# Kernel tuning notes

Measured on AMD Instinct MI355X. Metric: run time of the kernel, lower is better.

## Reference

```python
import jax, jax.numpy as jnp
import numpy as np

NEG_INF = -1e30

def _pool_unpool(x, k):
    # x: [B, C, H, W]. Non-overlapping max pool with window k (floor-mode,
    # matching torch MaxPool2d default), then MaxUnpool: scatter the pooled max
    # back to its argmax location within each window, zeros elsewhere.
    B, C, H, W = x.shape
    Hc, Wc = (H // k) * k, (W // k) * k  # cropped region covered by windows
    xc = x[:, :, :Hc, :Wc]
    # reshape into windows: [B, C, H/k, k, W/k, k] -> [B, C, H/k, W/k, k*k]
    xw = xc.reshape(B, C, Hc // k, k, Wc // k, k).transpose(0, 1, 2, 4, 3, 5)
    xw = xw.reshape(B, C, Hc // k, Wc // k, k * k)
    mx = jnp.max(xw, axis=-1, keepdims=True)
    am = jnp.argmax(xw, axis=-1)  # first max index, matches torch tie-breaking
    onehot = (jnp.arange(k * k) == am[..., None])
    yw = jnp.where(onehot, mx, jnp.zeros_like(mx))
    yc = yw.reshape(B, C, Hc // k, Wc // k, k, k).transpose(0, 1, 2, 4, 3, 5)
    yc = yc.reshape(B, C, Hc, Wc)
    # output_size=size in torch unpool -> pad uncovered border with zeros
    return jnp.pad(yc, ((0, 0), (0, 0), (0, H - Hc), (0, W - Wc)))

def setup_inputs() -> dict:
    key = jax.random.key(0)
    x = jax.random.uniform(key, (16, 1, 1080, 1920), dtype=jnp.float32)
    return {"x": x}

def reference(x):
    k = 3
    x = _pool_unpool(x, k)
    x = _pool_unpool(x, k + 2)
    x = _pool_unpool(x, k + 3)
    return x
```

## Files before the change

kernel.cpp:

```cpp
#include <hip/hip_runtime.h>


#define IMG_H 1080
#define IMG_W 1920
#define TILE_H 30
#define TILE_W 240
#define NTHREADS 256

template <int K>
__device__ __forceinline__ void nms_stage(float (*tile)[TILE_W], int t) {
    constexpr int NWR = TILE_H / K;
    constexpr int NWC = TILE_W / K;
    for (int w = t; w < NWR * NWC; w += NTHREADS) {
        const int wr = w / NWC;
        const int wc = w - wr * NWC;
        const int r0 = wr * K;
        const int c0 = wc * K;
        float mx = -1.0f;
        int am = 0;
#pragma unroll
        for (int r = 0; r < K; ++r)
#pragma unroll
            for (int c = 0; c < K; ++c) {
                const float v = tile[r0 + r][c0 + c];
                if (v > mx) { mx = v; am = r * K + c; }
            }
#pragma unroll
        for (int r = 0; r < K; ++r)
#pragma unroll
            for (int c = 0; c < K; ++c)
                tile[r0 + r][c0 + c] = (r * K + c == am) ? mx : 0.0f;
    }
    __syncthreads();
}

__global__ __launch_bounds__(NTHREADS) void pooling_nms_kernel(
    const float* __restrict__ x, float* __restrict__ out) {
    __shared__ float tile[TILE_H][TILE_W];

    const int t = threadIdx.x;
    const int col0 = blockIdx.x * TILE_W;
    const int row0 = blockIdx.y * TILE_H;
    const size_t base = (size_t)blockIdx.z * (IMG_H * (size_t)IMG_W) +
                        (size_t)row0 * IMG_W + col0;
    const float* src = x + base;
    float* dst = out + base;

    constexpr int VPR = TILE_W / 4;
    constexpr int NV = TILE_H * VPR;
    for (int i = t; i < NV; i += NTHREADS) {
        const int r = i / VPR;
        const int c4 = i - r * VPR;
        const float4 v =
            *reinterpret_cast<const float4*>(src + (size_t)r * IMG_W + c4 * 4);
        *reinterpret_cast<float4*>(&tile[r][c4 * 4]) = v;
    }
    __syncthreads();

    nms_stage<3>(tile, t);
    nms_stage<5>(tile, t);
    nms_stage<6>(tile, t);

    for (int i = t; i < NV; i += NTHREADS) {
        const int r = i / VPR;
        const int c4 = i - r * VPR;
        *reinterpret_cast<float4*>(dst + (size_t)r * IMG_W + c4 * 4) =
            *reinterpret_cast<const float4*>(&tile[r][c4 * 4]);
    }
}

extern "C" void kernel_launch(void* const* d_in, const int* in_sizes, int n_in,
                              void* d_out, int out_size, void* d_ws, size_t ws_size,
                              hipStream_t stream) {
    const float* x = (const float*)d_in[0];
    float* out = (float*)d_out;
    dim3 grid(IMG_W / TILE_W, IMG_H / TILE_H, 16);
    pooling_nms_kernel<<<grid, NTHREADS, 0, stream>>>(x, out);
}
```

Measured before the change: 238.8 us.

## Replace dense tile stages with sparse argmax-candidate cascade across pooling levels

Instead of staging the full tile in shared memory and rewriting it after each pool/unpool stage, the kernel computes 3x3 window maxima and positions directly from global memory. The 5x5 and 6x6 stages then operate only on sparse (value, position) candidates held in shared memory. The output tile is zero-filled and only the surviving maxima are scattered back. This removes the dense shared-memory read/write passes, at the cost of uncoalesced strided global reads and scattered single-element stores, plus added tie-breaking logic to stay exact.

```diff
diff --git a/kernel.cpp b/kernel.cpp
--- a/kernel.cpp
+++ b/kernel.cpp
@@ -5,67 +5,94 @@
 #define IMG_W 1920
 #define TILE_H 30
 #define TILE_W 240
-#define NTHREADS 256
+#define NT 256
 
-template <int K>
-__device__ __forceinline__ void nms_stage(float (*tile)[TILE_W], int t) {
-    constexpr int NWR = TILE_H / K;
-    constexpr int NWC = TILE_W / K;
-    for (int w = t; w < NWR * NWC; w += NTHREADS) {
-        const int wr = w / NWC;
-        const int wc = w - wr * NWC;
-        const int r0 = wr * K;
-        const int c0 = wc * K;
+__global__ __launch_bounds__(NT) void pooling_nms_kernel(
+    const float* __restrict__ x, float* __restrict__ out) {
+    __shared__ float sval[800];
+    __shared__ int   spos[800];
+    __shared__ float w5val[288];
+    __shared__ int   w5pos[288];
+
+    const int t = threadIdx.x;
+    const size_t base = (size_t)blockIdx.z * ((size_t)IMG_H * IMG_W) +
+                        (size_t)blockIdx.y * TILE_H * IMG_W +
+                        (size_t)blockIdx.x * TILE_W;
+    const float* src = x + base;
+    float* dst = out + base;
+
+    for (int w = t; w < 800; w += NT) {
+        const int wr = w / 80;
+        const int wc = w - wr * 80;
+        const int r0 = wr * 3, c0 = wc * 3;
         float mx = -1.0f;
         int am = 0;
 #pragma unroll
-        for (int r = 0; r < K; ++r)
-#pragma unroll
-            for (int c = 0; c < K; ++c) {
-                const float v = tile[r0 + r][c0 + c];
-                if (v > mx) { mx = v; am = r * K + c; }
-            }
-#pragma unroll
-        for (int r = 0; r < K; ++r)
-#pragma unroll
-            for (int c = 0; c < K; ++c)
-                tile[r0 + r][c0 + c] = (r * K + c == am) ? mx : 0.0f;
+        for (int r = 0; r < 3; ++r) {
+            const float* p = src + (size_t)(r0 + r) * IMG_W + c0;
+            const float v0 = p[0], v1 = p[1], v2 = p[2];
+            if (v0 > mx) { mx = v0; am = ((r0 + r) << 8) | c0; }
+            if (v1 > mx) { mx = v1; am = ((r0 + r) << 8) | (c0 + 1); }
+            if (v2 > mx) { mx = v2; am = ((r0 + r) << 8) | (c0 + 2); }
+        }
+        sval[w] = mx;
+        spos[w] = am;
     }
-    __syncthreads();
-}
 
-__global__ __launch_bounds__(NTHREADS) void pooling_nms_kernel(
-    const float* __restrict__ x, float* __restrict__ out) {
-    __shared__ float tile[TILE_H][TILE_W];
-
-    const int t = threadIdx.x;
-    const int col0 = blockIdx.x * TILE_W;
-    const int row0 = blockIdx.y * TILE_H;
-    const size_t base = (size_t)blockIdx.z * (IMG_H * (size_t)IMG_W) +
-                        (size_t)row0 * IMG_W + col0;
-    const float* src = x + base;
-    float* dst = out + base;
-
-    constexpr int VPR = TILE_W / 4;
-    constexpr int NV = TILE_H * VPR;
-    for (int i = t; i < NV; i += NTHREADS) {
-        const int r = i / VPR;
-        const int c4 = i - r * VPR;
-        const float4 v =
-            *reinterpret_cast<const float4*>(src + (size_t)r * IMG_W + c4 * 4);
-        *reinterpret_cast<float4*>(&tile[r][c4 * 4]) = v;
+    for (int i = t; i < (TILE_H * TILE_W / 4); i += NT) {
+        const int r = i / (TILE_W / 4);
+        const int c4 = i - r * (TILE_W / 4);
+        *reinterpret_cast<float4*>(dst + (size_t)r * IMG_W + c4 * 4) =
+            make_float4(0.f, 0.f, 0.f, 0.f);
     }
     __syncthreads();
 
-    nms_stage<3>(tile, t);
-    nms_stage<5>(tile, t);
-    nms_stage<6>(tile, t);
+    for (int w = t; w < 288; w += NT) {
+        const int a = w / 48;
+        const int b = w - a * 48;
+        const int rlo = (5 * a) / 3, rhi = (5 * a + 4) / 3;
+        const int clo = (5 * b) / 3, chi = (5 * b + 4) / 3;
+        float bv = -1.0f;
+        int bp = 0x7FFFFFFF;
+        for (int r3 = rlo; r3 <= rhi; ++r3)
+            for (int c3 = clo; c3 <= chi; ++c3) {
+                const int idx = r3 * 80 + c3;
+                const float v = sval[idx];
+                const int p = spos[idx];
+                const int r = p >> 8, c = p & 255;
+                const bool in =
+                    ((unsigned)(r - 5 * a) < 5u) & ((unsigned)(c - 5 * b) < 5u);
+                if (in && (v > bv || (v == bv && p < bp))) { bv = v; bp = p; }
+            }
+        w5val[w] = bv;
+        w5pos[w] = bp;
+    }
+    __syncthreads();
 
-    for (int i = t; i < NV; i += NTHREADS) {
-        const int r = i / VPR;
-        const int c4 = i - r * VPR;
-        *reinterpret_cast<float4*>(dst + (size_t)r * IMG_W + c4 * 4) =
-            *reinterpret_cast<const float4*>(&tile[r][c4 * 4]);
+    for (int w = t; w < 200; w += NT) {
+        const int a = w / 40;
+        const int b = w - a * 40;
+        const int rlo = (6 * a) / 5;
+        const int clo = (6 * b) / 5;
+        float bv = -1.0f;
+        int bp = 0x7FFFFFFF;
+#pragma unroll
+        for (int dr = 0; dr < 2; ++dr)
+#pragma unroll
+            for (int dc = 0; dc < 2; ++dc) {
+                const int idx = (rlo + dr) * 48 + (clo + dc);
+                const float v = w5val[idx];
+                const int p = w5pos[idx];
+                const int r = p >> 8, c = p & 255;
+                const bool in = (v >= 0.0f) &
+                                ((unsigned)(r - 6 * a) < 6u) &
+                                ((unsigned)(c - 6 * b) < 6u);
+                if (in && (v > bv || (v == bv && p < bp))) { bv = v; bp = p; }
+            }
+        if (bv >= 0.0f) {
+            const int r = bp >> 8, c = bp & 255;
+            dst[(size_t)r * IMG_W + c] = bv;
+        }
     }
 }
 
@@ -75,5 +102,5 @@
     const float* x = (const float*)d_in[0];
     float* out = (float*)d_out;
     dim3 grid(IMG_W / TILE_W, IMG_H / TILE_H, 16);
-    pooling_nms_kernel<<<grid, NTHREADS, 0, stream>>>(x, out);
+    pooling_nms_kernel<<<grid, NT, 0, stream>>>(x, out);
 }
```

Measured after the change: 255.0 us. 1.07x slower.
